# Performance work log

Hardware: AMD Instinct MI355X
Metric: run time of the kernel (lower is better)

Reference implementation:

```python
import jax, jax.numpy as jnp
import numpy as np

B, N, H, L, R, E = 8, 10000, 64, 4, 3, 200000
FP, NUM_CELLS = 2048, 100
LN_EPS = 1e-3  # Keras LayerNormalization default epsilon


def setup_inputs() -> dict:
    key = jax.random.key(0)
    ks = jax.random.split(key, 24)
    g = lambda k, shape, fan: (jax.random.uniform(k, shape, jnp.float32) * 2 - 1) * np.sqrt(6.0 / fan)
    inp = {
        'ctl_expr': jax.random.normal(ks[0], (B, N), jnp.float32),
        'drug_targets': jax.random.uniform(ks[1], (B, N), jnp.float32),
        'drug_fp': jax.random.uniform(ks[2], (B, FP), jnp.float32),
        'edge_weight': jax.random.uniform(ks[3], (R, E), jnp.float32),
        'cell_idx': jax.random.randint(ks[4], (B,), 0, NUM_CELLS, jnp.int32),
        'edge_index': jax.random.randint(ks[5], (R, 2, E), 0, N, jnp.int32),
        # parameters
        'W_se': g(ks[6], (1, H), 1 + H),
        'b_se': jnp.zeros((H,), jnp.float32),
        'cell_emb': jax.random.normal(ks[7], (NUM_CELLS, H), jnp.float32) * 0.05,
        'W_f1': g(ks[8], (FP, H), FP + H),
        'b_f1': jnp.zeros((H,), jnp.float32),
        'W_f2': g(ks[9], (H, 2 * H), 3 * H) * 0.1,
        'b_f2': jnp.zeros((2 * H,), jnp.float32),
        'Wself': jnp.stack([g(ks[10 + l], (H, H), 2 * H) for l in range(L)]),
        'Wrel': jnp.stack([jnp.stack([g(jax.random.fold_in(ks[14], l * R + r), (H, H), 2 * H) for r in range(R)]) for l in range(L)]),
        'ln_g': jnp.ones((L, H), jnp.float32),
        'ln_b': jnp.zeros((L, H), jnp.float32),
        'W_out': g(ks[15], (H, 1), H + 1),
        'b_out': jnp.zeros((1,), jnp.float32),
    }
    return inp


def reference(ctl_expr, drug_targets, drug_fp, edge_weight, cell_idx, edge_index,
              W_se, b_se, cell_emb, W_f1, b_f1, W_f2, b_f2,
              Wself, Wrel, ln_g, ln_b, W_out, b_out):
    # shared_embedding: Dense(H, relu) applied to scalar node features
    def shared(v):  # v: [B,N] -> [B,N,H]
        return jax.nn.relu(v[..., None] * W_se[0] + b_se)

    x = shared(ctl_expr) + shared(drug_targets)            # [B,N,H]
    x = x + cell_emb[cell_idx][:, None, :]                 # cell embedding broadcast

    # drug FiLM: gamma/beta conditioning
    film = jax.nn.relu(drug_fp @ W_f1 + b_f1) @ W_f2 + b_f2  # [B,2H]
    gamma, beta = jnp.split(film, 2, axis=-1)
    gamma = jnp.tanh(gamma)
    x = x * (1.0 + gamma[:, None, :]) + beta[:, None, :]

    n_layers, n_rel = Wself.shape[0], Wrel.shape[1]
    for l in range(n_layers):
        out = x @ Wself[l]                                 # self projection [B,N,H]
        for r in range(n_rel):
            src, dst = edge_index[r, 0], edge_index[r, 1]
            h = x @ Wrel[l, r]                             # [B,N,H]
            msg = edge_weight[r][None, :, None] * h[:, src, :]  # [B,E,H]
            out = out.at[:, dst].add(msg)                  # scatter-add to dst nodes
        # LayerNorm over feature dim (Keras eps=1e-3)
        mu = out.mean(-1, keepdims=True)
        var = ((out - mu) ** 2).mean(-1, keepdims=True)
        out = (out - mu) * jax.lax.rsqrt(var + LN_EPS) * ln_g[l] + ln_b[l]
        x = jax.nn.relu(out)

    return (x @ W_out)[..., 0] + b_out[0]                  # [B,N]
```

## Files before the change

kernel.cpp:

```cpp
#include <hip/hip_runtime.h>
#include <hip/hip_bf16.h>
#include <math.h>

#define Bk 8
#define Nk 10000
#define Hk 64
#define Lk 4
#define Rk 3
#define Ek 200000
#define FPk 2048

#define C4 (Rk*Ek/4)
#define CNT4B ((C4 + 255)/256)
#define INITB 2048

typedef unsigned short u16;
typedef unsigned int   u32;
typedef _Float16 f16;
typedef __attribute__((ext_vector_type(2))) _Float16 f16x2;
typedef __attribute__((ext_vector_type(8))) _Float16 f16x8;
typedef __attribute__((ext_vector_type(4))) float f32x4;

__device__ __forceinline__ f16x2 as_h2(u32 u){
    union{u32 i; f16x2 h;} v; v.i = u; return v.h;
}
__device__ __forceinline__ u32 as_u32(f16x2 h){
    union{u32 i; f16x2 h;} v; v.h = h; return v.i;
}
__device__ __forceinline__ u16 f2h_bits(float f){
    union{f16 h; u16 u;} v; v.h = (f16)f; return v.u;
}

__global__ void k_wprep(const float* __restrict__ Wself, const float* __restrict__ Wrel,
                        u16* __restrict__ wt, int* __restrict__ deg){
    int idx = blockIdx.x*256 + threadIdx.x;
    if(idx < Rk*Nk) deg[idx] = 0;
    if(idx >= Lk*4*2*4*64*8) return;
    int j    = idx & 7;
    int lane = (idx >> 3) & 63;
    int jt   = (idx >> 9) & 3;
    int kc   = (idx >> 11) & 1;
    int mt   = (idx >> 12) & 3;
    int l    = idx >> 14;
    int k    = kc*32 + (lane >> 4)*8 + j;
    int col  = jt*16 + (lane & 15);
    float w = (mt == 0) ? Wself[(l*64 + k)*64 + col]
                        : Wrel[((l*3 + (mt-1))*64 + k)*64 + col];
    wt[idx] = f2h_bits(w);
}

__global__ void k_count_film1(const int* __restrict__ edge_index, int* __restrict__ deg,
                              const float* __restrict__ fp, const float* __restrict__ W1,
                              const float* __restrict__ b1, float* __restrict__ hid){
    __shared__ float red[256];
    if(blockIdx.x < CNT4B){
        int idx = blockIdx.x*256 + threadIdx.x;
        if(idx >= C4) return;
        int g = idx*4;
        int r = g / Ek, e = g % Ek;
        int4 d = *(const int4*)&edge_index[r*2*Ek + Ek + e];
        int* dg = deg + r*Nk;
        atomicAdd(&dg[d.x], 1);
        atomicAdd(&dg[d.y], 1);
        atomicAdd(&dg[d.z], 1);
        atomicAdd(&dg[d.w], 1);
    }else{
        int bb = blockIdx.x - CNT4B;
        int b = bb >> 6, h = bb & 63;
        const float* fpb = fp + b*FPk;
        float acc = 0.f;
        for(int k = threadIdx.x; k < FPk; k += 256)
            acc += fpb[k] * W1[k*64 + h];
        red[threadIdx.x] = acc;
        __syncthreads();
        for(int s = 128; s >= 1; s >>= 1){
            if(threadIdx.x < s) red[threadIdx.x] += red[threadIdx.x + s];
            __syncthreads();
        }
        if(threadIdx.x == 0) hid[b*64 + h] = fmaxf(red[0] + b1[h], 0.f);
    }
}

__global__ void k_scan_film2(const int* __restrict__ deg, int* __restrict__ offs,
                             int* __restrict__ cursor,
                             const float* __restrict__ hid, const float* __restrict__ W2,
                             const float* __restrict__ b2,
                             float* __restrict__ g1p, float* __restrict__ beta){
    __shared__ int s[1024];
    if(blockIdx.x < 3){
        int r = blockIdx.x;
        int t = threadIdx.x;
        int base_i = t*10;
        int local[10];
        int sum = 0;
        if(base_i < Nk){
            #pragma unroll
            for(int k = 0; k < 10; ++k){ local[k] = deg[r*Nk + base_i + k]; sum += local[k]; }
        }
        s[t] = sum;
        __syncthreads();
        for(int d = 1; d < 1024; d <<= 1){
            int v = (t >= d) ? s[t-d] : 0;
            __syncthreads();
            s[t] += v;
            __syncthreads();
        }
        if(base_i < Nk){
            int excl = s[t] - sum;
            #pragma unroll
            for(int k = 0; k < 10; ++k){
                offs[r*(Nk+1) + base_i + k] = excl;
                cursor[r*Nk + base_i + k]   = excl;
                excl += local[k];
            }
        }
        if(t == 1023) offs[r*(Nk+1) + Nk] = s[1023];
    }else{
        int b = blockIdx.x - 3;
        int j = threadIdx.x;
        if(j < 128){
            float acc = b2[j];
            for(int k = 0; k < 64; ++k)
                acc += hid[b*64 + k] * W2[k*128 + j];
            if(j < 64) g1p[b*64 + j] = 1.f + tanhf(acc);
            else       beta[b*64 + j - 64] = acc;
        }
    }
}

__global__ void k_fill_init(const int* __restrict__ edge_index, const float* __restrict__ edge_weight,
                            int* __restrict__ cursor, int2* __restrict__ epack,
                            const float* __restrict__ ctl, const float* __restrict__ dt,
                            const int* __restrict__ cell_idx,
                            const float* __restrict__ W_se, const float* __restrict__ b_se,
                            const float* __restrict__ cell_emb,
                            const float* __restrict__ g1p, const float* __restrict__ beta,
                            u16* __restrict__ xh){
    if(blockIdx.x < CNT4B){
        int idx = blockIdx.x*256 + threadIdx.x;
        if(idx >= C4) return;
        int g = idx*4;
        int r = g / Ek, e = g % Ek;
        int4   s4 = *(const int4*)  &edge_index [r*2*Ek + e];
        int4   d4 = *(const int4*)  &edge_index [r*2*Ek + Ek + e];
        float4 w4 = *(const float4*)&edge_weight[r*Ek + e];
        int2* epr = epack + (size_t)r*Ek;
        int*  cur = cursor + r*Nk;
        int pos;
        f16 h;
        pos = atomicAdd(&cur[d4.x], 1); h = (f16)w4.x;
        epr[pos] = make_int2(s4.x << 7, (int)as_u32((f16x2){h, h}));
        pos = atomicAdd(&cur[d4.y], 1); h = (f16)w4.y;
        epr[pos] = make_int2(s4.y << 7, (int)as_u32((f16x2){h, h}));
        pos = atomicAdd(&cur[d4.z], 1); h = (f16)w4.z;
        epr[pos] = make_int2(s4.z << 7, (int)as_u32((f16x2){h, h}));
        pos = atomicAdd(&cur[d4.w], 1); h = (f16)w4.w;
        epr[pos] = make_int2(s4.w << 7, (int)as_u32((f16x2){h, h}));
    }else{
        const size_t total8 = (size_t)Bk*Nk*8;
        size_t start = (size_t)(blockIdx.x - CNT4B)*256 + threadIdx.x;
        for(size_t i8 = start; i8 < total8; i8 += (size_t)INITB*256){
            int hq = (int)(i8 & 7);
            size_t bn = i8 >> 3;
            int b = (int)(bn / Nk);
            float c = ctl[bn], d = dt[bn];
            int ci = cell_idx[b];
            u32 pk[4];
            #pragma unroll
            for(int j = 0; j < 8; j += 2){
                int h0 = hq*8 + j, h1 = h0 + 1;
                float w0 = W_se[h0], s0 = b_se[h0];
                float w1 = W_se[h1], s1 = b_se[h1];
                float v0 = fmaxf(c*w0 + s0, 0.f) + fmaxf(d*w0 + s0, 0.f)
                         + cell_emb[ci*64 + h0];
                float v1 = fmaxf(c*w1 + s1, 0.f) + fmaxf(d*w1 + s1, 0.f)
                         + cell_emb[ci*64 + h1];
                v0 = v0 * g1p[b*64 + h0] + beta[b*64 + h0];
                v1 = v1 * g1p[b*64 + h1] + beta[b*64 + h1];
                pk[j >> 1] = (u32)f2h_bits(v0) | ((u32)f2h_bits(v1) << 16);
            }
            *(int4*)&xh[i8*8] = make_int4(pk[0], pk[1], pk[2], pk[3]);
        }
    }
}

__global__ __launch_bounds__(256) void k_agg(const u16* __restrict__ xh,
                      const int* __restrict__ offs, const int2* __restrict__ epack,
                      u16* __restrict__ aggh){
    __shared__ int2 stash[4][64];
    int bpair = blockIdx.x & 3;
    int grp   = blockIdx.x >> 2;
    int wq    = threadIdx.x >> 6;
    int wid   = grp*4 + wq;
    int lane  = threadIdx.x & 63;
    int fg    = lane & 31;
    int bl    = lane >> 5;
    int b     = bpair*2 + bl;
    int r = wid / Nk, dst = wid % Nk;
    int o0 = offs[r*(Nk+1) + dst], o1 = offs[r*(Nk+1) + dst + 1];
    const int2* ep = epack + (size_t)r*Ek;
    const char* xb = (const char*)xh + (size_t)b*Nk*128 + fg*4;

    f16x2 A = (f16x2){0,0}, C = (f16x2){0,0};
    int2* st = stash[wq];
    for(int base = o0; base < o1; base += 64){
        int j = base + lane;
        if(j < o1) st[lane] = ep[j];
        int cnt = min(o1 - base, 64);
        int t = 0;
        for(; t + 16 <= cnt; t += 16){
            int4 q0 = *(const int4*)&st[t];
            int4 q1 = *(const int4*)&st[t+2];
            int4 q2 = *(const int4*)&st[t+4];
            int4 q3 = *(const int4*)&st[t+6];
            int4 q4 = *(const int4*)&st[t+8];
            int4 q5 = *(const int4*)&st[t+10];
            int4 q6 = *(const int4*)&st[t+12];
            int4 q7 = *(const int4*)&st[t+14];
            u32 u0 = *(const u32*)(xb + q0.x);
            u32 u1 = *(const u32*)(xb + q0.z);
            u32 u2 = *(const u32*)(xb + q1.x);
            u32 u3 = *(const u32*)(xb + q1.z);
            u32 u4 = *(const u32*)(xb + q2.x);
            u32 u5 = *(const u32*)(xb + q2.z);
            u32 u6 = *(const u32*)(xb + q3.x);
            u32 u7 = *(const u32*)(xb + q3.z);
            u32 u8 = *(const u32*)(xb + q4.x);
            u32 u9 = *(const u32*)(xb + q4.z);
            u32 ua = *(const u32*)(xb + q5.x);
            u32 ub = *(const u32*)(xb + q5.z);
            u32 uc = *(const u32*)(xb + q6.x);
            u32 ud = *(const u32*)(xb + q6.z);
            u32 ue = *(const u32*)(xb + q7.x);
            u32 uf = *(const u32*)(xb + q7.z);
            A += as_h2(u0)*as_h2(q0.y); C += as_h2(u1)*as_h2(q0.w);
            A += as_h2(u2)*as_h2(q1.y); C += as_h2(u3)*as_h2(q1.w);
            A += as_h2(u4)*as_h2(q2.y); C += as_h2(u5)*as_h2(q2.w);
            A += as_h2(u6)*as_h2(q3.y); C += as_h2(u7)*as_h2(q3.w);
            A += as_h2(u8)*as_h2(q4.y); C += as_h2(u9)*as_h2(q4.w);
            A += as_h2(ua)*as_h2(q5.y); C += as_h2(ub)*as_h2(q5.w);
            A += as_h2(uc)*as_h2(q6.y); C += as_h2(ud)*as_h2(q6.w);
            A += as_h2(ue)*as_h2(q7.y); C += as_h2(uf)*as_h2(q7.w);
        }
        for(; t + 8 <= cnt; t += 8){
            int4 q01 = *(const int4*)&st[t];
            int4 q23 = *(const int4*)&st[t+2];
            int4 q45 = *(const int4*)&st[t+4];
            int4 q67 = *(const int4*)&st[t+6];
            u32 u0 = *(const u32*)(xb + q01.x);
            u32 u1 = *(const u32*)(xb + q01.z);
            u32 u2 = *(const u32*)(xb + q23.x);
            u32 u3 = *(const u32*)(xb + q23.z);
            u32 u4 = *(const u32*)(xb + q45.x);
            u32 u5 = *(const u32*)(xb + q45.z);
            u32 u6 = *(const u32*)(xb + q67.x);
            u32 u7 = *(const u32*)(xb + q67.z);
            A += as_h2(u0)*as_h2(q01.y); C += as_h2(u1)*as_h2(q01.w);
            A += as_h2(u2)*as_h2(q23.y); C += as_h2(u3)*as_h2(q23.w);
            A += as_h2(u4)*as_h2(q45.y); C += as_h2(u5)*as_h2(q45.w);
            A += as_h2(u6)*as_h2(q67.y); C += as_h2(u7)*as_h2(q67.w);
        }
        for(; t + 2 <= cnt; t += 2){
            int4 q01 = *(const int4*)&st[t];
            u32 u0 = *(const u32*)(xb + q01.x);
            u32 u1 = *(const u32*)(xb + q01.z);
            A += as_h2(u0)*as_h2(q01.y); C += as_h2(u1)*as_h2(q01.w);
        }
        if(t < cnt){
            int2 p = st[t];
            u32 u = *(const u32*)(xb + p.x);
            A += as_h2(u)*as_h2(p.y);
        }
    }
    float a0 = (float)A.x + (float)C.x;
    float a1 = (float)A.y + (float)C.y;
    u32 packed = (u32)f2h_bits(a0) | ((u32)f2h_bits(a1) << 16);
    ((u32*)aggh)[(((size_t)r*Bk + b)*Nk + dst)*32 + fg] = packed;
}

__global__ __launch_bounds__(256) void k_proj_mfma(u16* __restrict__ xh,
        const u16* __restrict__ aggh, const u16* __restrict__ wt,
        const float* __restrict__ ln_g, const float* __restrict__ ln_b, int l,
        int last, const float* __restrict__ W_out, const float* __restrict__ b_out,
        float* __restrict__ out){
    int lane = threadIdx.x & 63;
    int wq   = threadIdx.x >> 6;
    int k8   = blockIdx.x & 7;
    int b    = ((k8 & 3) << 1) | (k8 >> 2);
    int tile = blockIdx.x >> 3;
    int n0   = tile*128 + wq*32;
    int mrow = lane & 15;
    int kq   = lane >> 4;
    int nA = n0 + mrow;       if(nA >= Nk) nA = Nk - 1;
    int nB = n0 + 16 + mrow;  if(nB >= Nk) nB = Nk - 1;

    f32x4 accA[4], accB[4];
    #pragma unroll
    for(int jt = 0; jt < 4; ++jt){
        accA[jt] = (f32x4){0.f,0.f,0.f,0.f};
        accB[jt] = (f32x4){0.f,0.f,0.f,0.f};
    }

    const u16* wl = wt + (size_t)l*16384;

    #pragma unroll
    for(int mt = 0; mt < 4; ++mt){
        const u16* basep = (mt == 0)
            ? xh   + (size_t)b*Nk*64
            : aggh + (((size_t)(mt-1)*Bk + b)*Nk)*64;
        const u16* arowA = basep + (size_t)nA*64;
        const u16* arowB = basep + (size_t)nB*64;
        #pragma unroll
        for(int kc = 0; kc < 2; ++kc){
            f16x8 aA = *(const f16x8*)(arowA + kc*32 + kq*8);
            f16x8 aB = *(const f16x8*)(arowB + kc*32 + kq*8);
            #pragma unroll
            for(int jt = 0; jt < 4; ++jt){
                size_t wi = ((size_t)((mt*2 + kc)*4 + jt)*64 + lane)*8;
                f16x8 bfrag = *(const f16x8*)(wl + wi);
                accA[jt] = __builtin_amdgcn_mfma_f32_16x16x32_f16(aA, bfrag, accA[jt], 0, 0, 0);
                accB[jt] = __builtin_amdgcn_mfma_f32_16x16x32_f16(aB, bfrag, accB[jt], 0, 0, 0);
            }
        }
    }

    float gv[4], bv[4], wo[4];
    #pragma unroll
    for(int jt = 0; jt < 4; ++jt){
        int f = jt*16 + mrow;
        gv[jt] = ln_g[l*64 + f];
        bv[jt] = ln_b[l*64 + f];
        wo[jt] = W_out[f];
    }
    float bo = b_out[0];
    u16* xdst = xh + (size_t)b*Nk*64;

    #pragma unroll
    for(int half = 0; half < 2; ++half){
        f32x4* acc = half ? accB : accA;
        int nbase = n0 + half*16;
        #pragma unroll
        for(int v = 0; v < 4; ++v){
            float s1 = acc[0][v] + acc[1][v] + acc[2][v] + acc[3][v];
            float s2 = acc[0][v]*acc[0][v] + acc[1][v]*acc[1][v]
                     + acc[2][v]*acc[2][v] + acc[3][v]*acc[3][v];
            #pragma unroll
            for(int off = 1; off <= 8; off <<= 1){
                s1 += __shfl_xor(s1, off);
                s2 += __shfl_xor(s2, off);
            }
            float mu  = s1 * 0.015625f;
            float var = s2 * 0.015625f - mu*mu;
            float rstd = rsqrtf(var + 1e-3f);
            int node = nbase + kq*4 + v;
            if(!last){
                if(node < Nk){
                    #pragma unroll
                    for(int jt = 0; jt < 4; ++jt){
                        float o = (acc[jt][v] - mu) * rstd * gv[jt] + bv[jt];
                        xdst[(size_t)node*64 + jt*16 + mrow] = f2h_bits(fmaxf(o, 0.f));
                    }
                }
            }else{
                float s3 = 0.f;
                #pragma unroll
                for(int jt = 0; jt < 4; ++jt){
                    float o = (acc[jt][v] - mu) * rstd * gv[jt] + bv[jt];
                    s3 += fmaxf(o, 0.f) * wo[jt];
                }
                #pragma unroll
                for(int off = 1; off <= 8; off <<= 1)
                    s3 += __shfl_xor(s3, off);
                if(mrow == 0 && node < Nk)
                    out[(size_t)b*Nk + node] = s3 + bo;
            }
        }
    }
}

extern "C" void kernel_launch(void* const* d_in, const int* in_sizes, int n_in,
                              void* d_out, int out_size, void* d_ws, size_t ws_size,
                              hipStream_t stream){
    const float* ctl        = (const float*)d_in[0];
    const float* dt         = (const float*)d_in[1];
    const float* drug_fp    = (const float*)d_in[2];
    const float* edge_w     = (const float*)d_in[3];
    const int*   cell_idx   = (const int*)  d_in[4];
    const int*   edge_index = (const int*)  d_in[5];
    const float* W_se       = (const float*)d_in[6];
    const float* b_se       = (const float*)d_in[7];
    const float* cell_emb   = (const float*)d_in[8];
    const float* W_f1       = (const float*)d_in[9];
    const float* b_f1       = (const float*)d_in[10];
    const float* W_f2       = (const float*)d_in[11];
    const float* b_f2       = (const float*)d_in[12];
    const float* Wself      = (const float*)d_in[13];
    const float* Wrel       = (const float*)d_in[14];
    const float* ln_g       = (const float*)d_in[15];
    const float* ln_b       = (const float*)d_in[16];
    const float* W_out      = (const float*)d_in[17];
    const float* b_out      = (const float*)d_in[18];
    float* out = (float*)d_out;

    char* p = (char*)d_ws;
    auto alloc = [&](size_t bytes)->char*{
        char* r = p; p += (bytes + 255) & ~(size_t)255; return r;
    };
    int*   deg    = (int*)  alloc((size_t)Rk*Nk*4);
    int*   cursor = (int*)  alloc((size_t)Rk*Nk*4);
    int*   offs   = (int*)  alloc((size_t)Rk*(Nk+1)*4);
    int2*  epack  = (int2*) alloc((size_t)Rk*Ek*8);
    float* hid    = (float*)alloc((size_t)Bk*64*4);
    float* g1p    = (float*)alloc((size_t)Bk*64*4);
    float* beta   = (float*)alloc((size_t)Bk*64*4);
    u16*   xh     = (u16*)  alloc((size_t)Bk*Nk*64*2);
    u16*   aggh   = (u16*)  alloc((size_t)3*Bk*Nk*64*2);
    u16*   wt     = (u16*)  alloc((size_t)Lk*16384*2);

    k_wprep<<<(Lk*4*2*4*64*8 + 255)/256, 256, 0, stream>>>(Wself, Wrel, wt, deg);

    k_count_film1<<<CNT4B + Bk*64, 256, 0, stream>>>(edge_index, deg, drug_fp, W_f1, b_f1, hid);
    k_scan_film2<<<3 + Bk, 1024, 0, stream>>>(deg, offs, cursor, hid, W_f2, b_f2, g1p, beta);
    k_fill_init<<<CNT4B + INITB, 256, 0, stream>>>(edge_index, edge_w, cursor, epack,
                                                   ctl, dt, cell_idx, W_se, b_se, cell_emb,
                                                   g1p, beta, xh);

    const int ntile = (Nk + 127)/128;
    for(int l = 0; l < Lk; ++l){
        k_agg<<<4*7500, 256, 0, stream>>>(xh, offs, epack, aggh);
        k_proj_mfma<<<ntile*8, 256, 0, stream>>>(
            xh, aggh, wt, ln_g, ln_b, l,
            (l == Lk-1) ? 1 : 0, W_out, b_out, out);
    }
}
```

Before: 412.9 us.

## Gather 16-byte feature chunks per lane and split edges across lane groups

Result: faster. 403.0 us (-2.4%).

```diff
diff --git a/kernel.cpp b/kernel.cpp
--- a/kernel.cpp
+++ b/kernel.cpp
@@ -193,89 +193,62 @@
     int wq    = threadIdx.x >> 6;
     int wid   = grp*4 + wq;
     int lane  = threadIdx.x & 63;
-    int fg    = lane & 31;
-    int bl    = lane >> 5;
-    int b     = bpair*2 + bl;
+    int eg    = lane >> 4;
+    int slot  = lane & 15;
+    int bl    = slot >> 3;
+    int fq    = slot & 7;
     int r = wid / Nk, dst = wid % Nk;
     int o0 = offs[r*(Nk+1) + dst], o1 = offs[r*(Nk+1) + dst + 1];
     const int2* ep = epack + (size_t)r*Ek;
-    const char* xb = (const char*)xh + (size_t)b*Nk*128 + fg*4;
-
-    f16x2 A = (f16x2){0,0}, C = (f16x2){0,0};
+    const char* xb = (const char*)xh + (size_t)(bpair*2 + bl)*Nk*128 + fq*16;
+
+    f16x2 a0 = (f16x2){0,0}, a1 = (f16x2){0,0};
+    f16x2 a2 = (f16x2){0,0}, a3 = (f16x2){0,0};
     int2* st = stash[wq];
     for(int base = o0; base < o1; base += 64){
         int j = base + lane;
         if(j < o1) st[lane] = ep[j];
         int cnt = min(o1 - base, 64);
         int t = 0;
-        for(; t + 16 <= cnt; t += 16){
-            int4 q0 = *(const int4*)&st[t];
-            int4 q1 = *(const int4*)&st[t+2];
-            int4 q2 = *(const int4*)&st[t+4];
-            int4 q3 = *(const int4*)&st[t+6];
-            int4 q4 = *(const int4*)&st[t+8];
-            int4 q5 = *(const int4*)&st[t+10];
-            int4 q6 = *(const int4*)&st[t+12];
-            int4 q7 = *(const int4*)&st[t+14];
-            u32 u0 = *(const u32*)(xb + q0.x);
-            u32 u1 = *(const u32*)(xb + q0.z);
-            u32 u2 = *(const u32*)(xb + q1.x);
-            u32 u3 = *(const u32*)(xb + q1.z);
-            u32 u4 = *(const u32*)(xb + q2.x);
-            u32 u5 = *(const u32*)(xb + q2.z);
-            u32 u6 = *(const u32*)(xb + q3.x);
-            u32 u7 = *(const u32*)(xb + q3.z);
-            u32 u8 = *(const u32*)(xb + q4.x);
-            u32 u9 = *(const u32*)(xb + q4.z);
-            u32 ua = *(const u32*)(xb + q5.x);
-            u32 ub = *(const u32*)(xb + q5.z);
-            u32 uc = *(const u32*)(xb + q6.x);
-            u32 ud = *(const u32*)(xb + q6.z);
-            u32 ue = *(const u32*)(xb + q7.x);
-            u32 uf = *(const u32*)(xb + q7.z);
-            A += as_h2(u0)*as_h2(q0.y); C += as_h2(u1)*as_h2(q0.w);
-            A += as_h2(u2)*as_h2(q1.y); C += as_h2(u3)*as_h2(q1.w);
-            A += as_h2(u4)*as_h2(q2.y); C += as_h2(u5)*as_h2(q2.w);
-            A += as_h2(u6)*as_h2(q3.y); C += as_h2(u7)*as_h2(q3.w);
-            A += as_h2(u8)*as_h2(q4.y); C += as_h2(u9)*as_h2(q4.w);
-            A += as_h2(ua)*as_h2(q5.y); C += as_h2(ub)*as_h2(q5.w);
-            A += as_h2(uc)*as_h2(q6.y); C += as_h2(ud)*as_h2(q6.w);
-            A += as_h2(ue)*as_h2(q7.y); C += as_h2(uf)*as_h2(q7.w);
-        }
         for(; t + 8 <= cnt; t += 8){
-            int4 q01 = *(const int4*)&st[t];
-            int4 q23 = *(const int4*)&st[t+2];
-            int4 q45 = *(const int4*)&st[t+4];
-            int4 q67 = *(const int4*)&st[t+6];
-            u32 u0 = *(const u32*)(xb + q01.x);
-            u32 u1 = *(const u32*)(xb + q01.z);
-            u32 u2 = *(const u32*)(xb + q23.x);
-            u32 u3 = *(const u32*)(xb + q23.z);
-            u32 u4 = *(const u32*)(xb + q45.x);
-            u32 u5 = *(const u32*)(xb + q45.z);
-            u32 u6 = *(const u32*)(xb + q67.x);
-            u32 u7 = *(const u32*)(xb + q67.z);
-            A += as_h2(u0)*as_h2(q01.y); C += as_h2(u1)*as_h2(q01.w);
-            A += as_h2(u2)*as_h2(q23.y); C += as_h2(u3)*as_h2(q23.w);
-            A += as_h2(u4)*as_h2(q45.y); C += as_h2(u5)*as_h2(q45.w);
-            A += as_h2(u6)*as_h2(q67.y); C += as_h2(u7)*as_h2(q67.w);
-        }
-        for(; t + 2 <= cnt; t += 2){
-            int4 q01 = *(const int4*)&st[t];
-            u32 u0 = *(const u32*)(xb + q01.x);
-            u32 u1 = *(const u32*)(xb + q01.z);
-            A += as_h2(u0)*as_h2(q01.y); C += as_h2(u1)*as_h2(q01.w);
-        }
-        if(t < cnt){
-            int2 p = st[t];
-            u32 u = *(const u32*)(xb + p.x);
-            A += as_h2(u)*as_h2(p.y);
-        }
-    }
-    float a0 = (float)A.x + (float)C.x;
-    float a1 = (float)A.y + (float)C.y;
-    u32 packed = (u32)f2h_bits(a0) | ((u32)f2h_bits(a1) << 16);
-    ((u32*)aggh)[(((size_t)r*Bk + b)*Nk + dst)*32 + fg] = packed;
+            int2 q0 = st[t + eg];
+            int2 q1 = st[t + 4 + eg];
+            int4 d0 = *(const int4*)(xb + q0.x);
+            int4 d1 = *(const int4*)(xb + q1.x);
+            f16x2 w0 = as_h2((u32)q0.y), w1 = as_h2((u32)q1.y);
+            a0 += as_h2((u32)d0.x)*w0; a1 += as_h2((u32)d0.y)*w0;
+            a2 += as_h2((u32)d0.z)*w0; a3 += as_h2((u32)d0.w)*w0;
+            a0 += as_h2((u32)d1.x)*w1; a1 += as_h2((u32)d1.y)*w1;
+            a2 += as_h2((u32)d1.z)*w1; a3 += as_h2((u32)d1.w)*w1;
+        }
+        for(; t < cnt; t += 4){
+            int idx = t + eg;
+            int2 q = st[min(idx, cnt - 1)];
+            u32 wbits = (idx < cnt) ? (u32)q.y : 0u;
+            int4 d = *(const int4*)(xb + q.x);
+            f16x2 w = as_h2(wbits);
+            a0 += as_h2((u32)d.x)*w; a1 += as_h2((u32)d.y)*w;
+            a2 += as_h2((u32)d.z)*w; a3 += as_h2((u32)d.w)*w;
+        }
+    }
+    float f0 = (float)a0.x, f1 = (float)a0.y, f2 = (float)a1.x, f3 = (float)a1.y;
+    float f4 = (float)a2.x, f5 = (float)a2.y, f6 = (float)a3.x, f7 = (float)a3.y;
+    f0 += __shfl_xor(f0, 16); f0 += __shfl_xor(f0, 32);
+    f1 += __shfl_xor(f1, 16); f1 += __shfl_xor(f1, 32);
+    f2 += __shfl_xor(f2, 16); f2 += __shfl_xor(f2, 32);
+    f3 += __shfl_xor(f3, 16); f3 += __shfl_xor(f3, 32);
+    f4 += __shfl_xor(f4, 16); f4 += __shfl_xor(f4, 32);
+    f5 += __shfl_xor(f5, 16); f5 += __shfl_xor(f5, 32);
+    f6 += __shfl_xor(f6, 16); f6 += __shfl_xor(f6, 32);
+    f7 += __shfl_xor(f7, 16); f7 += __shfl_xor(f7, 32);
+    if(eg == 0){
+        u32 p0 = (u32)f2h_bits(f0) | ((u32)f2h_bits(f1) << 16);
+        u32 p1 = (u32)f2h_bits(f2) | ((u32)f2h_bits(f3) << 16);
+        u32 p2 = (u32)f2h_bits(f4) | ((u32)f2h_bits(f5) << 16);
+        u32 p3 = (u32)f2h_bits(f6) | ((u32)f2h_bits(f7) << 16);
+        u16* dp = aggh + (((size_t)r*Bk + (bpair*2 + bl))*Nk + dst)*64 + fq*8;
+        *(int4*)dp = make_int4((int)p0, (int)p1, (int)p2, (int)p3);
+    }
 }
 
 __global__ __launch_bounds__(256) void k_proj_mfma(u16* __restrict__ xh,
```
